# Kernel tuning notes

Measured on AMD Instinct MI355X. Metric: run time of the kernel, lower is better.

Reference implementation:

```python
import jax, jax.numpy as jnp
import numpy as np

# fp4 e2m1 positive value grid and midpoints between adjacent grid values
_GRID = jnp.array([0.0, 0.5, 1.0, 1.5, 2.0, 3.0, 4.0, 6.0], dtype=jnp.float32)
_MIDS = jnp.array([0.25, 0.75, 1.25, 1.75, 2.5, 3.5, 5.0], dtype=jnp.float32)
BLOCK = 32               # MX block size
E8M0_BIAS = 127
F32_MIN_NORMAL = float(2.0 ** -126)
F4_E2M1_MAX_POW2 = 2     # log2 of largest power-of-two <= 6.0 -> 4.0


def _quantize_fp4(a):
    """Round-to-nearest-even onto the signed e2m1 grid."""
    mag = jnp.clip(jnp.abs(a), 0.0, 6.0)
    idx = jnp.searchsorted(_MIDS, mag, side='left')  # ties round down
    mids_pad = jnp.concatenate([_MIDS, jnp.array([-1.0], jnp.float32)])
    tie = mag == mids_pad[idx]
    idx = jnp.where(tie & (idx % 2 == 1), idx + 1, idx)  # ties-to-even mantissa
    return _GRID[idx] * jnp.where(a < 0, -1.0, 1.0)


def _floor_log2(m):
    """Exact floor(log2(m)) for m > 0, with corrections for fp rounding of log2."""
    e = jnp.floor(jnp.log2(m))
    e = jnp.where(jnp.exp2(e) > m, e - 1.0, e)
    e = jnp.where(jnp.exp2(e + 1.0) <= m, e + 1.0, e)
    return e


def _qdq_mxfp4(x):
    """Quantize-dequantize x to MX fp4_e2m1, block 32, FLOOR scale mode (to_mx + to_dtype)."""
    shp = x.shape
    xb = x.reshape(-1, BLOCK)
    max_abs = jnp.max(jnp.abs(xb), axis=1)
    eps = F32_MIN_NORMAL * (max_abs == 0).astype(jnp.float32)
    pow2 = _floor_log2(max_abs + eps)
    e_unb = jnp.clip(pow2 - F4_E2M1_MAX_POW2, -float(E8M0_BIAS), float(E8M0_BIAS) + 1.0)
    scale = jnp.maximum(jnp.exp2(e_unb), F32_MIN_NORMAL)  # [nblk]
    q = _quantize_fp4(xb / scale[:, None])
    return (q * scale[:, None]).reshape(shp)


def _dequant_weight(weight_packed, weight_scale, out_f, in_f):
    """Unpack uint8-packed fp4 (low nibble first), apply e8m0 block scales."""
    p = weight_packed.astype(jnp.int32)
    low = p & 0xF
    high = (p >> 4) & 0xF
    nib = jnp.stack([low, high], axis=-1).reshape(out_f, in_f)  # interleave low,high
    vals = _GRID[nib & 7] * jnp.where((nib & 8) > 0, -1.0, 1.0)
    s = jnp.exp2(weight_scale.astype(jnp.float32) - E8M0_BIAS)  # get_fp_scale(e8m0)
    return (vals.reshape(-1, BLOCK) * s[:, None]).reshape(out_f, in_f)


def setup_inputs() -> dict:
    key = jax.random.key(0)
    k1, k2, k3 = jax.random.split(key, 3)
    M, IN, OUT = 4096, 4096, 4096
    x = jax.random.normal(k1, (M, IN), dtype=jnp.float32)
    weight_packed = jax.random.randint(k2, (OUT, IN // 2), 0, 256, dtype=jnp.int32)
    weight_scale = jax.random.randint(k3, (OUT * IN // BLOCK,), 0, 135, dtype=jnp.int32)
    return {"x": x, "weight_packed": weight_packed, "weight_scale": weight_scale}


def reference(x, weight_packed, weight_scale):
    out_f = weight_packed.shape[0]
    in_f = weight_packed.shape[1] * 2
    xq = _qdq_mxfp4(x)                                       # qdq_mxfp4(x)
    w_dq = _dequant_weight(weight_packed, weight_scale, out_f, in_f)
    return xq @ w_dq.T                                       # matmul(x, w_dq.t())
```

## Files before the change

kernel.cpp:

```cpp
#include <hip/hip_runtime.h>
#include <stdint.h>

typedef __attribute__((ext_vector_type(4)))  int   intx4;
typedef __attribute__((ext_vector_type(8)))  int   intx8;
typedef __attribute__((ext_vector_type(16))) float floatx16;

#define GLL16(gp, lp)                                                               \
    __builtin_amdgcn_global_load_lds((const __attribute__((address_space(1))) unsigned int*)(gp), \
                                     (__attribute__((address_space(3))) unsigned int*)(lp), 16, 0, 0)
#define GLL4(gp, lp)                                                                \
    __builtin_amdgcn_global_load_lds((const __attribute__((address_space(1))) unsigned int*)(gp), \
                                     (__attribute__((address_space(3))) unsigned int*)(lp), 4, 0, 0)

__device__ __forceinline__ uint32_t enc1(float xv, float inv) {
    float a = fminf(fabsf(xv) * inv, 6.0f);
    int e;
    if (a < 2.0f)      e = (int)rintf(a + a);
    else if (a < 4.0f) e = (int)rintf(a) + 2;
    else               e = (int)rintf(a * 0.5f) + 4;
    return (uint32_t)e | ((__float_as_uint(xv) >> 28) & 8u);
}

__global__ __launch_bounds__(256) void quant_x_kernel(const float* __restrict__ x,
                                                      uint32_t* __restrict__ xq,
                                                      uint8_t* __restrict__ xs) {
    int t = blockIdx.x * 256 + threadIdx.x;
    const float4* src = (const float4*)(x + (size_t)t * 8);
    float4 v0 = src[0], v1 = src[1];
    float mx = fmaxf(fmaxf(fmaxf(fabsf(v0.x), fabsf(v0.y)), fmaxf(fabsf(v0.z), fabsf(v0.w))),
                     fmaxf(fmaxf(fabsf(v1.x), fabsf(v1.y)), fmaxf(fabsf(v1.z), fabsf(v1.w))));
    mx = fmaxf(mx, __shfl_xor(mx, 1, 64));
    mx = fmaxf(mx, __shfl_xor(mx, 2, 64));
    unsigned ef = __float_as_uint(mx) >> 23;
    unsigned code = (ef < 3u) ? 1u : (ef - 2u);
    float inv = __uint_as_float((254u - code) << 23);

    uint32_t w =  enc1(v0.x, inv)        | (enc1(v0.y, inv) << 4)
               | (enc1(v0.z, inv) << 8)  | (enc1(v0.w, inv) << 12)
               | (enc1(v1.x, inv) << 16) | (enc1(v1.y, inv) << 20)
               | (enc1(v1.z, inv) << 24) | (enc1(v1.w, inv) << 28);
    xq[t] = w;
    if ((threadIdx.x & 3) == 0) xs[t >> 2] = (uint8_t)code;
}

__global__ __launch_bounds__(256) void repack_kernel(const int* __restrict__ wp,
                                                     const int* __restrict__ wsc,
                                                     uint32_t* __restrict__ wrep,
                                                     uint32_t* __restrict__ wscb,
                                                     int n4w, int n4s) {
    int t = blockIdx.x * 256 + threadIdx.x;
    if (t < n4w) {
        int4 p = ((const int4*)wp)[t];
        wrep[t] = (uint32_t)(p.x & 0xFF) | ((uint32_t)(p.y & 0xFF) << 8)
                | ((uint32_t)(p.z & 0xFF) << 16) | ((uint32_t)(p.w & 0xFF) << 24);
    } else if (t - n4w < n4s) {
        int u = t - n4w;
        int4 p = ((const int4*)wsc)[u];
        wscb[u] = (uint32_t)(p.x & 0xFF) | ((uint32_t)(p.y & 0xFF) << 8)
                | ((uint32_t)(p.z & 0xFF) << 16) | ((uint32_t)(p.w & 0xFF) << 24);
    }
}

__global__ __launch_bounds__(256, 1) void gemm_mx_kernel(const uint8_t* __restrict__ Apk,
                                                         const uint8_t* __restrict__ Bpk,
                                                         const uint8_t* __restrict__ As,
                                                         const uint8_t* __restrict__ Bs,
                                                         float* __restrict__ C,
                                                         int M, int N, int K) {
    __shared__ __align__(16) uint8_t sA[2][16384];
    __shared__ __align__(16) uint8_t sB[2][16384];
    __shared__ __align__(16) uint8_t sAs[2][1024];
    __shared__ __align__(16) uint8_t sBs[2][1024];

    const int tid = threadIdx.x;
    const int bm0 = blockIdx.y << 8;
    const int bn0 = blockIdx.x << 8;
    const int wave = tid >> 6;
    const int lane = tid & 63;
    const int wm = (wave >> 1) << 7;
    const int wn = (wave & 1) << 7;
    const int row = lane & 31;
    const int h = lane >> 5;
    const int Kb = K >> 1;
    const int kbpr = K >> 5;

    int soff[4];
    const uint8_t* Aga[4];
    const uint8_t* Bga[4];
#pragma unroll
    for (int i = 0; i < 4; ++i) {
        int s = tid + 256 * i;
        int r = s >> 2;
        int p = (s & 3) ^ ((r >> 1) & 3);
        soff[i] = s * 16;
        Aga[i] = Apk + (size_t)(bm0 + r) * Kb + p * 16;
        Bga[i] = Bpk + (size_t)(bn0 + r) * Kb + p * 16;
    }
    const uint8_t* Asg = As + (size_t)(bm0 + tid) * kbpr;
    const uint8_t* Bsg = Bs + (size_t)(bn0 + tid) * kbpr;

    floatx16 acc[4][4];
#pragma unroll
    for (int a = 0; a < 4; ++a)
#pragma unroll
        for (int b = 0; b < 4; ++b)
#pragma unroll
            for (int r = 0; r < 16; ++r) acc[a][b][r] = 0.f;

    const int nchunk = K >> 7;

#pragma unroll
    for (int i = 0; i < 4; ++i) {
        GLL16(Aga[i], sA[0] + soff[i]);
        GLL16(Bga[i], sB[0] + soff[i]);
    }
    GLL4(Asg, sAs[0] + tid * 4);
    GLL4(Bsg, sBs[0] + tid * 4);

    for (int c = 0; c < nchunk; ++c) {
        const int buf = c & 1;
        __syncthreads();
        if (c + 1 < nchunk) {
            const int nb = buf ^ 1;
            const size_t koff = (size_t)(c + 1) * 64;
#pragma unroll
            for (int i = 0; i < 4; ++i) {
                GLL16(Aga[i] + koff, sA[nb] + soff[i]);
                GLL16(Bga[i] + koff, sB[nb] + soff[i]);
            }
            GLL4(Asg + (c + 1) * 4, sAs[nb] + tid * 4);
            GLL4(Bsg + (c + 1) * 4, sBs[nb] + tid * 4);
        }

#pragma unroll
        for (int s = 0; s < 2; ++s) {
            const int kp = 2 * s + h;
            intx4 a4[4], b4[4];
            int sa[4], sb[4];
#pragma unroll
            for (int mt = 0; mt < 4; ++mt) {
                const int lr = wm + mt * 32 + row;
                a4[mt] = *(const intx4*)(sA[buf] + (lr * 4 + (kp ^ ((lr >> 1) & 3))) * 16);
                sa[mt] = sAs[buf][lr * 4 + kp];
            }
#pragma unroll
            for (int nt = 0; nt < 4; ++nt) {
                const int lr = wn + nt * 32 + row;
                b4[nt] = *(const intx4*)(sB[buf] + (lr * 4 + (kp ^ ((lr >> 1) & 3))) * 16);
                sb[nt] = sBs[buf][lr * 4 + kp];
            }
#pragma unroll
            for (int mt = 0; mt < 4; ++mt)
#pragma unroll
                for (int nt = 0; nt < 4; ++nt) {
                    intx8 a8 = {a4[mt][0], a4[mt][1], a4[mt][2], a4[mt][3], 0, 0, 0, 0};
                    intx8 b8 = {b4[nt][0], b4[nt][1], b4[nt][2], b4[nt][3], 0, 0, 0, 0};
                    acc[mt][nt] = __builtin_amdgcn_mfma_scale_f32_32x32x64_f8f6f4(
                        a8, b8, acc[mt][nt], 4, 4, 0, sa[mt], 0, sb[nt]);
                }
        }
    }

#pragma unroll
    for (int mt = 0; mt < 4; ++mt)
#pragma unroll
        for (int nt = 0; nt < 4; ++nt) {
            const int col = bn0 + wn + nt * 32 + row;
#pragma unroll
            for (int g = 0; g < 4; ++g) {
                const int rw = bm0 + wm + mt * 32 + 8 * g + 4 * h;
#pragma unroll
                for (int q = 0; q < 4; ++q)
                    C[(size_t)(rw + q) * N + col] = acc[mt][nt][4 * g + q];
            }
        }
}

extern "C" void kernel_launch(void* const* d_in, const int* in_sizes, int n_in,
                              void* d_out, int out_size, void* d_ws, size_t ws_size,
                              hipStream_t stream) {
    const float* x = (const float*)d_in[0];
    const int* wp = (const int*)d_in[1];
    const int* wsc = (const int*)d_in[2];
    float* out = (float*)d_out;

    const int K = 4096;
    const int M = in_sizes[0] / K;
    const int N = (in_sizes[1] * 2) / K;
    const int kbpr = K / 32;
    const int npack = N * K / 2;
    const int nsc = N * kbpr;

    uint32_t* xq   = (uint32_t*)d_ws;
    uint8_t*  xs   = (uint8_t*)d_ws + (size_t)M * K / 2;
    uint32_t* wrep = (uint32_t*)(xs + (size_t)M * kbpr);
    uint8_t*  wscb = (uint8_t*)wrep + (size_t)npack;

    quant_x_kernel<<<(M * K / 8) / 256, 256, 0, stream>>>(x, xq, xs);

    int n4w = npack / 4, n4s = nsc / 4;
    repack_kernel<<<(n4w + n4s + 255) / 256, 256, 0, stream>>>(wp, wsc, wrep,
                                                               (uint32_t*)wscb, n4w, n4s);

    dim3 grid(N / 256, M / 256);
    gemm_mx_kernel<<<grid, 256, 0, stream>>>((const uint8_t*)xq, (const uint8_t*)wrep,
                                             xs, wscb, out, M, N, K);
}
```

Before: 208.7 us.

## Use per-wave private LDS staging with vmcnt waits and 128x128 tiles

After: 293.0 us. 40.4% more time.

```diff
diff --git a/kernel.cpp b/kernel.cpp
--- a/kernel.cpp
+++ b/kernel.cpp
@@ -11,6 +11,9 @@
 #define GLL4(gp, lp)                                                                \
     __builtin_amdgcn_global_load_lds((const __attribute__((address_space(1))) unsigned int*)(gp), \
                                      (__attribute__((address_space(3))) unsigned int*)(lp), 4, 0, 0)
+
+#define WAITV10 asm volatile("s_waitcnt vmcnt(10)" ::: "memory")
+#define WAITV0  asm volatile("s_waitcnt vmcnt(0)"  ::: "memory")
 
 __device__ __forceinline__ uint32_t enc1(float xv, float inv) {
     float a = fminf(fabsf(xv) * inv, 6.0f);
@@ -61,98 +64,96 @@
     }
 }
 
-__global__ __launch_bounds__(256, 1) void gemm_mx_kernel(const uint8_t* __restrict__ Apk,
+__global__ __launch_bounds__(256, 2) void gemm_mx_kernel(const uint8_t* __restrict__ Apk,
                                                          const uint8_t* __restrict__ Bpk,
                                                          const uint8_t* __restrict__ As,
                                                          const uint8_t* __restrict__ Bs,
                                                          float* __restrict__ C,
                                                          int M, int N, int K) {
-    __shared__ __align__(16) uint8_t sA[2][16384];
-    __shared__ __align__(16) uint8_t sB[2][16384];
-    __shared__ __align__(16) uint8_t sAs[2][1024];
-    __shared__ __align__(16) uint8_t sBs[2][1024];
+    __shared__ __align__(16) uint8_t lds[4][2][8704];
 
     const int tid = threadIdx.x;
-    const int bm0 = blockIdx.y << 8;
-    const int bn0 = blockIdx.x << 8;
     const int wave = tid >> 6;
     const int lane = tid & 63;
-    const int wm = (wave >> 1) << 7;
-    const int wn = (wave & 1) << 7;
     const int row = lane & 31;
     const int h = lane >> 5;
+    const int bm0 = blockIdx.y << 7;
+    const int bn0 = blockIdx.x << 7;
+    const int wm = (wave >> 1) << 6;
+    const int wn = (wave & 1) << 6;
     const int Kb = K >> 1;
     const int kbpr = K >> 5;
 
-    int soff[4];
-    const uint8_t* Aga[4];
-    const uint8_t* Bga[4];
-#pragma unroll
-    for (int i = 0; i < 4; ++i) {
-        int s = tid + 256 * i;
-        int r = s >> 2;
-        int p = (s & 3) ^ ((r >> 1) & 3);
-        soff[i] = s * 16;
-        Aga[i] = Apk + (size_t)(bm0 + r) * Kb + p * 16;
-        Bga[i] = Bpk + (size_t)(bn0 + r) * Kb + p * 16;
-    }
-    const uint8_t* Asg = As + (size_t)(bm0 + tid) * kbpr;
-    const uint8_t* Bsg = Bs + (size_t)(bn0 + tid) * kbpr;
-
-    floatx16 acc[4][4];
-#pragma unroll
-    for (int a = 0; a < 4; ++a)
-#pragma unroll
-        for (int b = 0; b < 4; ++b)
+    const uint8_t* Agp[4];
+    const uint8_t* Bgp[4];
+#pragma unroll
+    for (int g = 0; g < 4; ++g) {
+        const int s = g >> 1, mt = g & 1;
+        const int r = mt * 32 + row;
+        const int kp = 2 * s + h;
+        Agp[g] = Apk + (size_t)(bm0 + wm + r) * Kb + kp * 16;
+        Bgp[g] = Bpk + (size_t)(bn0 + wn + r) * Kb + kp * 16;
+    }
+    const uint8_t* Asp = As + (size_t)(bm0 + wm + lane) * kbpr;
+    const uint8_t* Bsp = Bs + (size_t)(bn0 + wn + lane) * kbpr;
+
+    uint8_t* reg0 = lds[wave][0];
+    uint8_t* reg1 = lds[wave][1];
+
+    floatx16 acc[2][2];
+#pragma unroll
+    for (int a = 0; a < 2; ++a)
+#pragma unroll
+        for (int b = 0; b < 2; ++b)
 #pragma unroll
             for (int r = 0; r < 16; ++r) acc[a][b][r] = 0.f;
 
     const int nchunk = K >> 7;
 
 #pragma unroll
-    for (int i = 0; i < 4; ++i) {
-        GLL16(Aga[i], sA[0] + soff[i]);
-        GLL16(Bga[i], sB[0] + soff[i]);
-    }
-    GLL4(Asg, sAs[0] + tid * 4);
-    GLL4(Bsg, sBs[0] + tid * 4);
+    for (int g = 0; g < 4; ++g) {
+        GLL16(Agp[g], reg0 + (g * 64 + lane) * 16);
+        GLL16(Bgp[g], reg0 + 4096 + (g * 64 + lane) * 16);
+    }
+    GLL4(Asp, reg0 + 8192 + lane * 4);
+    GLL4(Bsp, reg0 + 8448 + lane * 4);
 
     for (int c = 0; c < nchunk; ++c) {
-        const int buf = c & 1;
-        __syncthreads();
+        uint8_t* cur = (c & 1) ? reg1 : reg0;
+        uint8_t* nxt = (c & 1) ? reg0 : reg1;
         if (c + 1 < nchunk) {
-            const int nb = buf ^ 1;
             const size_t koff = (size_t)(c + 1) * 64;
 #pragma unroll
-            for (int i = 0; i < 4; ++i) {
-                GLL16(Aga[i] + koff, sA[nb] + soff[i]);
-                GLL16(Bga[i] + koff, sB[nb] + soff[i]);
-            }
-            GLL4(Asg + (c + 1) * 4, sAs[nb] + tid * 4);
-            GLL4(Bsg + (c + 1) * 4, sBs[nb] + tid * 4);
+            for (int g = 0; g < 4; ++g) {
+                GLL16(Agp[g] + koff, nxt + (g * 64 + lane) * 16);
+                GLL16(Bgp[g] + koff, nxt + 4096 + (g * 64 + lane) * 16);
+            }
+            GLL4(Asp + (c + 1) * 4, nxt + 8192 + lane * 4);
+            GLL4(Bsp + (c + 1) * 4, nxt + 8448 + lane * 4);
+            WAITV10;
+        } else {
+            WAITV0;
         }
 
 #pragma unroll
         for (int s = 0; s < 2; ++s) {
+            intx4 a4[2], b4[2];
+            int sa[2], sb[2];
             const int kp = 2 * s + h;
-            intx4 a4[4], b4[4];
-            int sa[4], sb[4];
-#pragma unroll
-            for (int mt = 0; mt < 4; ++mt) {
-                const int lr = wm + mt * 32 + row;
-                a4[mt] = *(const intx4*)(sA[buf] + (lr * 4 + (kp ^ ((lr >> 1) & 3))) * 16);
-                sa[mt] = sAs[buf][lr * 4 + kp];
-            }
-#pragma unroll
-            for (int nt = 0; nt < 4; ++nt) {
-                const int lr = wn + nt * 32 + row;
-                b4[nt] = *(const intx4*)(sB[buf] + (lr * 4 + (kp ^ ((lr >> 1) & 3))) * 16);
-                sb[nt] = sBs[buf][lr * 4 + kp];
-            }
-#pragma unroll
-            for (int mt = 0; mt < 4; ++mt)
-#pragma unroll
-                for (int nt = 0; nt < 4; ++nt) {
+#pragma unroll
+            for (int mt = 0; mt < 2; ++mt) {
+                a4[mt] = *(const intx4*)(cur + ((s * 2 + mt) * 64 + lane) * 16);
+                sa[mt] = cur[8192 + (mt * 32 + row) * 4 + kp];
+            }
+#pragma unroll
+            for (int nt = 0; nt < 2; ++nt) {
+                b4[nt] = *(const intx4*)(cur + 4096 + ((s * 2 + nt) * 64 + lane) * 16);
+                sb[nt] = cur[8448 + (nt * 32 + row) * 4 + kp];
+            }
+#pragma unroll
+            for (int mt = 0; mt < 2; ++mt)
+#pragma unroll
+                for (int nt = 0; nt < 2; ++nt) {
                     intx8 a8 = {a4[mt][0], a4[mt][1], a4[mt][2], a4[mt][3], 0, 0, 0, 0};
                     intx8 b8 = {b4[nt][0], b4[nt][1], b4[nt][2], b4[nt][3], 0, 0, 0, 0};
                     acc[mt][nt] = __builtin_amdgcn_mfma_scale_f32_32x32x64_f8f6f4(
@@ -162,9 +163,9 @@
     }
 
 #pragma unroll
-    for (int mt = 0; mt < 4; ++mt)
-#pragma unroll
-        for (int nt = 0; nt < 4; ++nt) {
+    for (int mt = 0; mt < 2; ++mt)
+#pragma unroll
+        for (int nt = 0; nt < 2; ++nt) {
             const int col = bn0 + wn + nt * 32 + row;
 #pragma unroll
             for (int g = 0; g < 4; ++g) {
@@ -202,7 +203,7 @@
     repack_kernel<<<(n4w + n4s + 255) / 256, 256, 0, stream>>>(wp, wsc, wrep,
                                                                (uint32_t*)wscb, n4w, n4s);
 
-    dim3 grid(N / 256, M / 256);
+    dim3 grid(N / 128, M / 128);
     gemm_mx_kernel<<<grid, 256, 0, stream>>>((const uint8_t*)xq, (const uint8_t*)wrep,
                                              xs, wscb, out, M, N, K);
 }
```
